# Kernel tuning notes

Measured on AMD Instinct MI355X. Metric: run time of the kernel, lower is better.

## Reference

```python
import jax, jax.numpy as jnp
import numpy as np

EMB, BS, H = 512, 1024, 8
HD = EMB // H
B, L = 8, 1024
EPS = 1e-5

def setup_inputs() -> dict:
    key = jax.random.key(0)
    ks = jax.random.split(key, 12)
    s = EMB ** -0.5
    return {
        "x": jax.random.normal(ks[0], (B, L, EMB), jnp.float32),
        "ln_g": jnp.ones((EMB,), jnp.float32),
        "ln_b": jnp.zeros((EMB,), jnp.float32),
        "Wq": jax.random.normal(ks[1], (EMB, EMB), jnp.float32) * s,
        "bq": jnp.zeros((EMB,), jnp.float32),
        "Wk": jax.random.normal(ks[2], (EMB, EMB), jnp.float32) * s,
        "bk": jnp.zeros((EMB,), jnp.float32),
        "Wv": jax.random.normal(ks[3], (EMB, EMB), jnp.float32) * s,
        "bv": jnp.zeros((EMB,), jnp.float32),
        "Wo": jax.random.normal(ks[4], (EMB, EMB), jnp.float32) * s,
        "bo": jnp.zeros((EMB,), jnp.float32),
        "Er": jax.random.normal(ks[5], (H, BS, HD), jnp.float32),
    }

def reference(x, ln_g, ln_b, Wq, bq, Wk, bk, Wv, bv, Wo, bo, Er):
    b, l, d = x.shape
    # LayerNorm
    mu = jnp.mean(x, axis=-1, keepdims=True)
    var = jnp.mean((x - mu) ** 2, axis=-1, keepdims=True)
    h = (x - mu) * jax.lax.rsqrt(var + EPS) * ln_g + ln_b
    # projections -> (B, H, L, HD)
    def split_heads(t):
        return t.reshape(b, l, H, HD).transpose(0, 2, 1, 3)
    q = split_heads(h @ Wq + bq)
    k = split_heads(h @ Wk + bk)
    v = split_heads(h @ Wv + bv)
    scores = jnp.einsum('bhld,bhkd->bhlk', q, k) * (HD ** -0.5)
    # relative bias: QEr_all[b,h,l,r] = q . Er[h,r]; then gather r = (k - l) mod BS
    QEr_all = jnp.einsum('bhld,hrd->bhlr', q, Er)  # (B,H,L,BS)
    rel = (jnp.arange(l)[None, :] - jnp.arange(l)[:, None]) % BS  # (L,L), torch negative-index wrap
    QEr = jnp.take_along_axis(QEr_all, rel[None, None], axis=-1)  # (B,H,L,L)
    w = jax.nn.softmax(scores + QEr, axis=-1)
    out = jnp.einsum('bhlk,bhkd->bhld', w, v)
    out = out.transpose(0, 2, 1, 3).reshape(b, l, d)
    return out @ Wo + bo
```

## Files before the change

kernel.cpp:

```cpp
#include <hip/hip_runtime.h>
#include <hip/hip_bf16.h>


typedef __bf16 bf16;
typedef __bf16 bf16x8 __attribute__((ext_vector_type(8)));
typedef float floatx4 __attribute__((ext_vector_type(4)));
typedef float f32x4 __attribute__((ext_vector_type(4)));

#define MFMA16 __builtin_amdgcn_mfma_f32_16x16x32_bf16

#define KS 72
#define BSS 83
#define PSS 68
#define GS 40

__global__ __launch_bounds__(256) void prep_ln_kernel(
    const float* __restrict__ Wq, const float* __restrict__ Wk,
    const float* __restrict__ Wv, const float* __restrict__ Wo,
    const float* __restrict__ Er,
    const float* __restrict__ x, const float* __restrict__ g,
    const float* __restrict__ bvec,
    bf16* __restrict__ wt, bf16* __restrict__ er_b, bf16* __restrict__ h) {
  int blk = blockIdx.x;
  if (blk < 6144) {
    int idx = blk * 256 + threadIdx.x;
    if (idx < 4 * 512 * 512) {
      int w = idx >> 18;
      int r = idx & 262143;
      int n = r >> 9, k = r & 511;
      const float* W = (w == 0) ? Wq : (w == 1) ? Wk : (w == 2) ? Wv : Wo;
      wt[idx] = (bf16)W[k * 512 + n];
    } else {
      int e = idx - 4 * 512 * 512;
      er_b[e] = (bf16)Er[e];
    }
    return;
  }
  int row = (blk - 6144) * 4 + (threadIdx.x >> 6);
  int lane = threadIdx.x & 63;
  const f32x4* xr = (const f32x4*)(x + row * 512 + lane * 8);
  f32x4 v0 = xr[0], v1 = xr[1];
  float f[8] = {v0[0], v0[1], v0[2], v0[3], v1[0], v1[1], v1[2], v1[3]};
  float s = 0.f, ss = 0.f;
#pragma unroll
  for (int i = 0; i < 8; i++) { s += f[i]; ss += f[i] * f[i]; }
#pragma unroll
  for (int m = 1; m < 64; m <<= 1) { s += __shfl_xor(s, m); ss += __shfl_xor(ss, m); }
  float mean = s * (1.0f / 512.0f);
  float var = ss * (1.0f / 512.0f) - mean * mean;
  float inv = rsqrtf(var + 1e-5f);
  const f32x4* gr = (const f32x4*)(g + lane * 8);
  const f32x4* br = (const f32x4*)(bvec + lane * 8);
  f32x4 g0 = gr[0], g1 = gr[1], b0 = br[0], b1 = br[1];
  float gg[8] = {g0[0], g0[1], g0[2], g0[3], g1[0], g1[1], g1[2], g1[3]};
  float bb[8] = {b0[0], b0[1], b0[2], b0[3], b1[0], b1[1], b1[2], b1[3]};
  bf16x8 o;
#pragma unroll
  for (int i = 0; i < 8; i++)
    o[i] = (bf16)((f[i] - mean) * inv * gg[i] + bb[i]);
  *(bf16x8*)(h + row * 512 + lane * 8) = o;
}


__global__ __launch_bounds__(256) void qkv_gemm(
    const bf16* __restrict__ A,
    const bf16* __restrict__ wt,
    const float* __restrict__ bq, const float* __restrict__ bk,
    const float* __restrict__ bv,
    bf16* __restrict__ q_ws, bf16* __restrict__ k_ws, bf16* __restrict__ vt_ws) {
  __shared__ __align__(16) bf16 As[128 * GS];
  __shared__ __align__(16) bf16 Bs[128 * GS];
  int m0 = blockIdx.x * 128;
  int ng0 = blockIdx.y * 128;
  int w = ng0 >> 9;
  int n0 = ng0 & 511;
  const bf16* Bt = wt + (w << 18);
  int tid = threadIdx.x;
  int wave = tid >> 6, lane = tid & 63, quad = lane >> 4, l16 = lane & 15;
  int mq = (wave >> 1) * 64, nq = (wave & 1) * 64;

  floatx4 acc[4][4] = {};
  for (int k0 = 0; k0 < 512; k0 += 32) {
    int r = tid >> 1, c = (tid & 1) * 16;
    *(bf16x8*)(As + r * GS + c)     = *(const bf16x8*)(A + (m0 + r) * 512 + k0 + c);
    *(bf16x8*)(As + r * GS + c + 8) = *(const bf16x8*)(A + (m0 + r) * 512 + k0 + c + 8);
    *(bf16x8*)(Bs + r * GS + c)     = *(const bf16x8*)(Bt + (n0 + r) * 512 + k0 + c);
    *(bf16x8*)(Bs + r * GS + c + 8) = *(const bf16x8*)(Bt + (n0 + r) * 512 + k0 + c + 8);
    __syncthreads();
    bf16x8 a[4], b[4];
#pragma unroll
    for (int mt = 0; mt < 4; mt++)
      a[mt] = *(const bf16x8*)(As + (mq + mt * 16 + l16) * GS + quad * 8);
#pragma unroll
    for (int nt = 0; nt < 4; nt++)
      b[nt] = *(const bf16x8*)(Bs + (nq + nt * 16 + l16) * GS + quad * 8);
#pragma unroll
    for (int mt = 0; mt < 4; mt++)
#pragma unroll
      for (int nt = 0; nt < 4; nt++)
        acc[mt][nt] = MFMA16(a[mt], b[nt], acc[mt][nt], 0, 0, 0);
    __syncthreads();
  }

  const float* bias = (w == 0) ? bq : (w == 1) ? bk : bv;
#pragma unroll
  for (int nt = 0; nt < 4; nt++) {
    int col = n0 + nq + nt * 16 + l16;
    float bb = bias[col];
    int hh = col >> 6, d = col & 63;
#pragma unroll
    for (int mt = 0; mt < 4; mt++) {
#pragma unroll
      for (int r = 0; r < 4; r++) {
        int mrow = m0 + mq + mt * 16 + quad * 4 + r;
        int b_ = mrow >> 10, l = mrow & 1023;
        int bh = b_ * 8 + hh;
        float v = acc[mt][nt][r] + bb;
        if (w == 0)       q_ws[(bh << 16) + (l << 6) + d] = (bf16)v;
        else if (w == 1)  k_ws[(bh << 16) + (l << 6) + d] = (bf16)(v * 0.125f);
        else              vt_ws[(bh << 16) + (d << 10) + l] = (bf16)v;
      }
    }
  }
}

__global__ __launch_bounds__(256, 2) void attn_kernel(
    const bf16* __restrict__ q_ws, const bf16* __restrict__ k_ws,
    const bf16* __restrict__ vt_ws, const bf16* __restrict__ Er,
    bf16* __restrict__ o_ws) {
  __shared__ __align__(16) bf16 Ks_s[64 * KS];
  __shared__ __align__(16) bf16 Vs[64 * KS];
  __shared__ __align__(16) bf16 Ers[192 * KS];
  __shared__ __align__(16) float bias_s[4][16 * BSS];
  __shared__ __align__(16) bf16 Ps[4][16 * PSS];

  int qt = blockIdx.x;
  int bh = blockIdx.y;
  int hh = bh & 7;
  int l0 = qt << 7;
  int tid = threadIdx.x, wave = tid >> 6, lane = tid & 63;
  int quad = lane >> 4, l16 = lane & 15;

  bf16x8 aq0[2], aq1[2];
#pragma unroll
  for (int strip = 0; strip < 2; strip++) {
    const bf16* qb = q_ws + (bh << 16) + ((l0 + strip * 64 + wave * 16 + l16) << 6);
    aq0[strip] = *(const bf16x8*)(qb + quad * 8);
    aq1[strip] = *(const bf16x8*)(qb + 32 + quad * 8);
  }

  const bf16* kbh = k_ws + (bh << 16);
  const bf16* vbh = vt_ws + (bh << 16);
  const bf16* ebh = Er + (hh << 16);
  float* bw = bias_s[wave];
  bf16* pw = Ps[wave];

  float l_run[2][4] = {};
  floatx4 acc_o[2][4] = {};

  int e0 = -l0 - 127 + 2048;

  for (int kt = 0; kt < 16; kt++) {
    int k0 = kt * 64;
#pragma unroll
    for (int i = 0; i < 2; i++) {
      int o = tid + i * 256;
      int row = o >> 3, ch = (o & 7) * 8;
      *(bf16x8*)(Ks_s + row * KS + ch) =
          *(const bf16x8*)(kbh + ((k0 + row) << 6) + ch);
      *(bf16x8*)(Vs + row * KS + ch) =
          *(const bf16x8*)(vbh + (row << 10) + k0 + ch);
    }
#pragma unroll
    for (int i = 0; i < 6; i++) {
      int o = tid + i * 256;
      int row = o >> 3, ch = (o & 7) * 8;
      int grow = (e0 + k0 + row) & 1023;
      *(bf16x8*)(Ers + row * KS + ch) =
          *(const bf16x8*)(ebh + (grow << 6) + ch);
    }
    __syncthreads();

    bf16x8 kb0[4], kb1[4], vb0[4], vb1[4];
#pragma unroll
    for (int nt = 0; nt < 4; nt++) {
      const bf16* kr = Ks_s + (nt * 16 + l16) * KS + quad * 8;
      kb0[nt] = *(const bf16x8*)kr;
      kb1[nt] = *(const bf16x8*)(kr + 32);
      const bf16* vr = Vs + (nt * 16 + l16) * KS + quad * 8;
      vb0[nt] = *(const bf16x8*)vr;
      vb1[nt] = *(const bf16x8*)(vr + 32);
    }

#pragma unroll
    for (int strip = 0; strip < 2; strip++) {
      floatx4 acc_s[4] = {};
#pragma unroll
      for (int nt = 0; nt < 4; nt++) {
        acc_s[nt] = MFMA16(aq0[strip], kb0[nt], acc_s[nt], 0, 0, 0);
        acc_s[nt] = MFMA16(aq1[strip], kb1[nt], acc_s[nt], 0, 0, 0);
      }
      int t0 = (strip ? 3 : 7) - wave;
#pragma unroll
      for (int nt2 = 0; nt2 < 5; nt2++) {
        int erow = (t0 + nt2) * 16 + l16;
        const bf16* er = Ers + erow * KS + quad * 8;
        bf16x8 b0 = *(const bf16x8*)er;
        bf16x8 b1 = *(const bf16x8*)(er + 32);
        floatx4 accb = {};
        accb = MFMA16(aq0[strip], b0, accb, 0, 0, 0);
        accb = MFMA16(aq1[strip], b1, accb, 0, 0, 0);
#pragma unroll
        for (int r = 0; r < 4; r++)
          bw[(quad * 4 + r) * BSS + nt2 * 16 + l16] = accb[r];
      }
      float pv[4][4];
#pragma unroll
      for (int nt = 0; nt < 4; nt++) {
        int dk = nt * 16 + l16;
#pragma unroll
        for (int r = 0; r < 4; r++) {
          int sdl = quad * 4 + r;
          float sc = acc_s[nt][r] + bw[sdl * BSS + 15 + dk - sdl];
          pv[nt][r] = __expf(sc);
        }
      }
#pragma unroll
      for (int r = 0; r < 4; r++)
        l_run[strip][r] += pv[0][r] + pv[1][r] + pv[2][r] + pv[3][r];
#pragma unroll
      for (int nt = 0; nt < 4; nt++)
#pragma unroll
        for (int r = 0; r < 4; r++)
          pw[(quad * 4 + r) * PSS + nt * 16 + l16] = (bf16)pv[nt][r];
      bf16x8 ap0 = *(const bf16x8*)(pw + l16 * PSS + quad * 8);
      bf16x8 ap1 = *(const bf16x8*)(pw + l16 * PSS + 32 + quad * 8);
#pragma unroll
      for (int dt = 0; dt < 4; dt++) {
        acc_o[strip][dt] = MFMA16(ap0, vb0[dt], acc_o[strip][dt], 0, 0, 0);
        acc_o[strip][dt] = MFMA16(ap1, vb1[dt], acc_o[strip][dt], 0, 0, 0);
      }
    }
    __syncthreads();
  }

#pragma unroll
  for (int strip = 0; strip < 2; strip++) {
    float invl[4];
#pragma unroll
    for (int r = 0; r < 4; r++) {
      float lr = l_run[strip][r];
#pragma unroll
      for (int m = 1; m < 16; m <<= 1) lr += __shfl_xor(lr, m);
      invl[r] = 1.0f / lr;
    }
#pragma unroll
    for (int dt = 0; dt < 4; dt++) {
      int col = (hh << 6) + dt * 16 + l16;
#pragma unroll
      for (int r = 0; r < 4; r++) {
        int row = ((bh >> 3) << 10) + l0 + strip * 64 + wave * 16 + quad * 4 + r;
        o_ws[row * 512 + col] = (bf16)(acc_o[strip][dt][r] * invl[r]);
      }
    }
  }
}

__global__ __launch_bounds__(256) void out_gemm(
    const bf16* __restrict__ A,
    const bf16* __restrict__ Bt,
    const float* __restrict__ bo, float* __restrict__ out) {
  __shared__ __align__(16) bf16 As[128 * GS];
  __shared__ __align__(16) bf16 Bs[128 * GS];
  int m0 = blockIdx.x * 128;
  int n0 = blockIdx.y * 128;
  int tid = threadIdx.x;
  int wave = tid >> 6, lane = tid & 63, quad = lane >> 4, l16 = lane & 15;
  int mq = (wave >> 1) * 64, nq = (wave & 1) * 64;

  floatx4 acc[4][4] = {};
  for (int k0 = 0; k0 < 512; k0 += 32) {
    int r = tid >> 1, c = (tid & 1) * 16;
    *(bf16x8*)(As + r * GS + c)     = *(const bf16x8*)(A + (m0 + r) * 512 + k0 + c);
    *(bf16x8*)(As + r * GS + c + 8) = *(const bf16x8*)(A + (m0 + r) * 512 + k0 + c + 8);
    *(bf16x8*)(Bs + r * GS + c)     = *(const bf16x8*)(Bt + (n0 + r) * 512 + k0 + c);
    *(bf16x8*)(Bs + r * GS + c + 8) = *(const bf16x8*)(Bt + (n0 + r) * 512 + k0 + c + 8);
    __syncthreads();
    bf16x8 a[4], b[4];
#pragma unroll
    for (int mt = 0; mt < 4; mt++)
      a[mt] = *(const bf16x8*)(As + (mq + mt * 16 + l16) * GS + quad * 8);
#pragma unroll
    for (int nt = 0; nt < 4; nt++)
      b[nt] = *(const bf16x8*)(Bs + (nq + nt * 16 + l16) * GS + quad * 8);
#pragma unroll
    for (int mt = 0; mt < 4; mt++)
#pragma unroll
      for (int nt = 0; nt < 4; nt++)
        acc[mt][nt] = MFMA16(a[mt], b[nt], acc[mt][nt], 0, 0, 0);
    __syncthreads();
  }
#pragma unroll
  for (int nt = 0; nt < 4; nt++) {
    int col = n0 + nq + nt * 16 + l16;
    float bb = bo[col];
#pragma unroll
    for (int mt = 0; mt < 4; mt++) {
#pragma unroll
      for (int r = 0; r < 4; r++) {
        int mrow = m0 + mq + mt * 16 + quad * 4 + r;
        out[mrow * 512 + col] = acc[mt][nt][r] + bb;
      }
    }
  }
}

extern "C" void kernel_launch(void* const* d_in, const int* in_sizes, int n_in,
                              void* d_out, int out_size, void* d_ws, size_t ws_size,
                              hipStream_t stream) {
  const float* x    = (const float*)d_in[0];
  const float* ln_g = (const float*)d_in[1];
  const float* ln_b = (const float*)d_in[2];
  const float* Wq   = (const float*)d_in[3];
  const float* bq   = (const float*)d_in[4];
  const float* Wk   = (const float*)d_in[5];
  const float* bk   = (const float*)d_in[6];
  const float* Wv   = (const float*)d_in[7];
  const float* bv   = (const float*)d_in[8];
  const float* Wo   = (const float*)d_in[9];
  const float* bo   = (const float*)d_in[10];
  const float* Er   = (const float*)d_in[11];
  float* out = (float*)d_out;

  char* ws = (char*)d_ws;
  bf16* wt    = (bf16*)(ws);
  bf16* er_b  = (bf16*)(ws + (2u << 20));
  bf16* h     = (bf16*)(ws + (3u << 20));
  bf16* o_ws  = h;
  bf16* q_ws  = (bf16*)(ws + (11u << 20));
  bf16* k_ws  = (bf16*)(ws + (19u << 20));
  bf16* vt_ws = (bf16*)(ws + (27u << 20));

  prep_ln_kernel<<<8192, 256, 0, stream>>>(Wq, Wk, Wv, Wo, Er, x, ln_g, ln_b,
                                           wt, er_b, h);
  qkv_gemm<<<dim3(64, 12), 256, 0, stream>>>(h, wt, bq, bk, bv, q_ws, k_ws, vt_ws);
  attn_kernel<<<dim3(8, 64), 256, 0, stream>>>(q_ws, k_ws, vt_ws, er_b, o_ws);
  out_gemm<<<dim3(64, 4), 256, 0, stream>>>(o_ws, wt + 3 * 262144, bo, out);
}
```

Before: 216.6 us.

## Tile weight transpose through LDS, stage V transpose, reuse Er ring buffer

The weight cast-and-transpose now goes through an LDS tile, so both global reads and writes are coalesced instead of strided scalar reads. The Er cast gets its own blocks. The V-transposed output of the QKV GEMM is staged in shared memory so each thread writes 16-byte contiguous chunks instead of scattered 2-byte stores. The attention kernel keeps Er rows in a 12-slot ring buffer and loads only 64 new rows per key tile instead of reloading all 192. The P buffer stride also changes from 68 to 72. This adds index bookkeeping and a larger shared-memory footprint in qkv_gemm.

```diff
diff --git a/kernel.cpp b/kernel.cpp
--- a/kernel.cpp
+++ b/kernel.cpp
@@ -11,8 +11,9 @@
 
 #define KS 72
 #define BSS 83
-#define PSS 68
+#define PSS 72
 #define GS 40
+#define TS 72
 
 __global__ __launch_bounds__(256) void prep_ln_kernel(
     const float* __restrict__ Wq, const float* __restrict__ Wk,
@@ -21,23 +22,38 @@
     const float* __restrict__ x, const float* __restrict__ g,
     const float* __restrict__ bvec,
     bf16* __restrict__ wt, bf16* __restrict__ er_b, bf16* __restrict__ h) {
+  __shared__ __align__(16) bf16 T[64 * TS];
   int blk = blockIdx.x;
-  if (blk < 6144) {
-    int idx = blk * 256 + threadIdx.x;
-    if (idx < 4 * 512 * 512) {
-      int w = idx >> 18;
-      int r = idx & 262143;
-      int n = r >> 9, k = r & 511;
-      const float* W = (w == 0) ? Wq : (w == 1) ? Wk : (w == 2) ? Wv : Wo;
-      wt[idx] = (bf16)W[k * 512 + n];
-    } else {
-      int e = idx - 4 * 512 * 512;
-      er_b[e] = (bf16)Er[e];
-    }
+  int tid = threadIdx.x;
+  if (blk < 256) {
+    int w = blk >> 6, rem = blk & 63;
+    int r0 = (rem >> 3) << 6, c0 = (rem & 7) << 6;
+    const float* W = (w == 0) ? Wq : (w == 1) ? Wk : (w == 2) ? Wv : Wo;
+    int row = tid >> 2, cc = (tid & 3) << 4;
+    const f32x4* src = (const f32x4*)(W + (r0 + row) * 512 + c0 + cc);
+#pragma unroll
+    for (int q2 = 0; q2 < 4; q2++) {
+      f32x4 v = src[q2];
+#pragma unroll
+      for (int j = 0; j < 4; j++)
+        T[(cc + q2 * 4 + j) * TS + row] = (bf16)v[j];
+    }
+    __syncthreads();
+    int nloc = tid >> 2, kc = (tid & 3) << 4;
+    bf16x8 a = *(const bf16x8*)(T + nloc * TS + kc);
+    bf16x8 b = *(const bf16x8*)(T + nloc * TS + kc + 8);
+    bf16* dst = wt + (w << 18) + (c0 + nloc) * 512 + r0 + kc;
+    *(bf16x8*)dst = a;
+    *(bf16x8*)(dst + 8) = b;
     return;
   }
-  int row = (blk - 6144) * 4 + (threadIdx.x >> 6);
-  int lane = threadIdx.x & 63;
+  if (blk < 2304) {
+    int e = (blk - 256) * 256 + tid;
+    er_b[e] = (bf16)Er[e];
+    return;
+  }
+  int row = (blk - 2304) * 4 + (tid >> 6);
+  int lane = tid & 63;
   const f32x4* xr = (const f32x4*)(x + row * 512 + lane * 8);
   f32x4 v0 = xr[0], v1 = xr[1];
   float f[8] = {v0[0], v0[1], v0[2], v0[3], v1[0], v1[1], v1[2], v1[3]};
@@ -68,8 +84,9 @@
     const float* __restrict__ bq, const float* __restrict__ bk,
     const float* __restrict__ bv,
     bf16* __restrict__ q_ws, bf16* __restrict__ k_ws, bf16* __restrict__ vt_ws) {
-  __shared__ __align__(16) bf16 As[128 * GS];
-  __shared__ __align__(16) bf16 Bs[128 * GS];
+  __shared__ __align__(16) bf16 smem[64 * 264];
+  bf16* As = smem;
+  bf16* Bs = smem + 128 * GS;
   int m0 = blockIdx.x * 128;
   int ng0 = blockIdx.y * 128;
   int w = ng0 >> 9;
@@ -102,7 +119,37 @@
     __syncthreads();
   }
 
-  const float* bias = (w == 0) ? bq : (w == 1) ? bk : bv;
+  if (w == 2) {
+#pragma unroll
+    for (int nt = 0; nt < 4; nt++) {
+      int col = n0 + nq + nt * 16 + l16;
+      float bb = bv[col];
+      int d = col & 63;
+#pragma unroll
+      for (int mt = 0; mt < 4; mt++)
+#pragma unroll
+        for (int r = 0; r < 4; r++) {
+          int lloc = mq + mt * 16 + quad * 4 + r;
+          smem[d * 264 + (wave & 1) * 128 + lloc] = (bf16)(acc[mt][nt][r] + bb);
+        }
+    }
+    __syncthreads();
+    int b_ = m0 >> 10, l0g = m0 & 1023;
+    int dloc = tid >> 4, lc = (tid & 15) * 8;
+#pragma unroll
+    for (int h2 = 0; h2 < 2; h2++) {
+      int bh = b_ * 8 + ((n0 + h2 * 64) >> 6);
+#pragma unroll
+      for (int dd = 0; dd < 4; dd++) {
+        int d = dd * 16 + dloc;
+        bf16x8 v = *(const bf16x8*)(smem + d * 264 + h2 * 128 + lc);
+        *(bf16x8*)(vt_ws + (bh << 16) + (d << 10) + l0g + lc) = v;
+      }
+    }
+    return;
+  }
+
+  const float* bias = (w == 0) ? bq : bk;
 #pragma unroll
   for (int nt = 0; nt < 4; nt++) {
     int col = n0 + nq + nt * 16 + l16;
@@ -116,9 +163,8 @@
         int b_ = mrow >> 10, l = mrow & 1023;
         int bh = b_ * 8 + hh;
         float v = acc[mt][nt][r] + bb;
-        if (w == 0)       q_ws[(bh << 16) + (l << 6) + d] = (bf16)v;
-        else if (w == 1)  k_ws[(bh << 16) + (l << 6) + d] = (bf16)(v * 0.125f);
-        else              vt_ws[(bh << 16) + (d << 10) + l] = (bf16)v;
+        if (w == 0) q_ws[(bh << 16) + (l << 6) + d] = (bf16)v;
+        else        k_ws[(bh << 16) + (l << 6) + d] = (bf16)(v * 0.125f);
       }
     }
   }
@@ -159,6 +205,14 @@
   floatx4 acc_o[2][4] = {};
 
   int e0 = -l0 - 127 + 2048;
+#pragma unroll
+  for (int i = 0; i < 4; i++) {
+    int o = tid + i * 256;
+    int row = o >> 3, ch = (o & 7) * 8;
+    int grow = (e0 + row) & 1023;
+    *(bf16x8*)(Ers + row * KS + ch) = *(const bf16x8*)(ebh + (grow << 6) + ch);
+  }
+  int sb = 0;
 
   for (int kt = 0; kt < 16; kt++) {
     int k0 = kt * 64;
@@ -171,13 +225,17 @@
       *(bf16x8*)(Vs + row * KS + ch) =
           *(const bf16x8*)(vbh + (row << 10) + k0 + ch);
     }
-#pragma unroll
-    for (int i = 0; i < 6; i++) {
-      int o = tid + i * 256;
-      int row = o >> 3, ch = (o & 7) * 8;
-      int grow = (e0 + k0 + row) & 1023;
-      *(bf16x8*)(Ers + row * KS + ch) =
-          *(const bf16x8*)(ebh + (grow << 6) + ch);
+    {
+      int s8 = sb + 8; if (s8 >= 12) s8 -= 12;
+      int srow0 = s8 << 4;
+#pragma unroll
+      for (int i = 0; i < 2; i++) {
+        int o = tid + i * 256;
+        int row = o >> 3, ch = (o & 7) * 8;
+        int grow = (e0 + 128 + k0 + row) & 1023;
+        *(bf16x8*)(Ers + (srow0 + row) * KS + ch) =
+            *(const bf16x8*)(ebh + (grow << 6) + ch);
+      }
     }
     __syncthreads();
 
@@ -203,8 +261,8 @@
       int t0 = (strip ? 3 : 7) - wave;
 #pragma unroll
       for (int nt2 = 0; nt2 < 5; nt2++) {
-        int erow = (t0 + nt2) * 16 + l16;
-        const bf16* er = Ers + erow * KS + quad * 8;
+        int tt = sb + t0 + nt2; if (tt >= 12) tt -= 12;
+        const bf16* er = Ers + ((tt << 4) + l16) * KS + quad * 8;
         bf16x8 b0 = *(const bf16x8*)er;
         bf16x8 b1 = *(const bf16x8*)(er + 32);
         floatx4 accb = {};
@@ -241,6 +299,7 @@
         acc_o[strip][dt] = MFMA16(ap1, vb1[dt], acc_o[strip][dt], 0, 0, 0);
       }
     }
+    sb += 4; if (sb >= 12) sb -= 12;
     __syncthreads();
   }
 
@@ -341,7 +400,7 @@
   bf16* k_ws  = (bf16*)(ws + (19u << 20));
   bf16* vt_ws = (bf16*)(ws + (27u << 20));
 
-  prep_ln_kernel<<<8192, 256, 0, stream>>>(Wq, Wk, Wv, Wo, Er, x, ln_g, ln_b,
+  prep_ln_kernel<<<4352, 256, 0, stream>>>(Wq, Wk, Wv, Wo, Er, x, ln_g, ln_b,
                                            wt, er_b, h);
   qkv_gemm<<<dim3(64, 12), 256, 0, stream>>>(h, wt, bq, bk, bv, q_ws, k_ws, vt_ws);
   attn_kernel<<<dim3(8, 64), 256, 0, stream>>>(q_ws, k_ws, vt_ws, er_b, o_ws);
```

New measurement: 201.3 us. 1.08x faster.
